# Kernel optimization log

Hardware: AMD Instinct MI355X
Metric: run time of the kernel (lower is better)

The kernel has to match this reference:

```python
import jax, jax.numpy as jnp
import numpy as np

N, E, F, H, L, G, C, NC = 100000, 1200000, 32, 64, 3, 256, 200000, 10
D = L * H  # concat node embedding dim = 192


def setup_inputs() -> dict:
    key = jax.random.key(0)
    ks = jax.random.split(key, 20)

    def w(k, shape):
        fan_in = shape[-2] if len(shape) > 1 else shape[0]
        return jax.random.normal(k, shape, jnp.float32) * (1.0 / np.sqrt(fan_in))

    inp = dict(
        x=jax.random.normal(ks[0], (N, F), jnp.float32),
        edge_index=jax.random.randint(ks[1], (2, E), 0, N),
        batch=jnp.sort(jax.random.randint(ks[2], (N,), 0, G)),
        cand_node=jax.random.randint(ks[3], (C,), 0, N),
        c1_W1=w(ks[4], (F, H)), c1_b1=jnp.zeros((H,)),
        c1_W2=w(ks[5], (H, H)), c1_b2=jnp.zeros((H,)),
        c1_g=jnp.ones((H,)), c1_be=jnp.zeros((H,)), c1_m=jnp.zeros((H,)), c1_v=jnp.ones((H,)),
        c1_eps=jnp.zeros((1,)),
        cs_W1=w(ks[6], (L - 1, H, H)), cs_b1=jnp.zeros((L - 1, H)),
        cs_W2=w(ks[7], (L - 1, H, H)), cs_b2=jnp.zeros((L - 1, H)),
        cs_g=jnp.ones((L - 1, H)), cs_be=jnp.zeros((L - 1, H)),
        cs_m=jnp.zeros((L - 1, H)), cs_v=jnp.ones((L - 1, H)),
        cs_eps=jnp.zeros((L - 1,)),
        nc_W1=w(ks[8], (D, 2 * H)), nc_b1=jnp.zeros((2 * H,)),
        nc_W2=w(ks[9], (2 * H, H)), nc_b2=jnp.zeros((H,)),
        nc_W3=w(ks[10], (H, H)), nc_b3=jnp.zeros((H,)),
        nc_W4=w(ks[11], (H, NC)), nc_b4=jnp.zeros((NC,)),
        comp_emb=jax.random.normal(ks[12], (NC, D), jnp.float32),
        ep_W1=w(ks[13], (2 * D, 2 * H)), ep_b1=jnp.zeros((2 * H,)),
        ep_W2=w(ks[14], (2 * H, H)), ep_b2=jnp.zeros((H,)),
        ep_W3=w(ks[15], (H, 1)), ep_b3=jnp.zeros((1,)),
    )
    return inp


def _bn(h, g, b, m, v):
    # BatchNorm1d in eval mode with running stats
    return g * (h - m) * jax.lax.rsqrt(v + 1e-5) + b


def _gin_layer(h, src, dst, eps, W1, b1, W2, b2, g, be, m, v):
    agg = jax.ops.segment_sum(h[src], dst, num_segments=N)  # sum aggregation
    h = (1.0 + eps) * h + agg
    h = jax.nn.relu(h @ W1 + b1)
    h = jax.nn.relu(h @ W2 + b2)
    return _bn(h, g, be, m, v)


def reference(x, edge_index, batch, cand_node,
              c1_W1, c1_b1, c1_W2, c1_b2, c1_g, c1_be, c1_m, c1_v, c1_eps,
              cs_W1, cs_b1, cs_W2, cs_b2, cs_g, cs_be, cs_m, cs_v, cs_eps,
              nc_W1, nc_b1, nc_W2, nc_b2, nc_W3, nc_b3, nc_W4, nc_b4,
              comp_emb, ep_W1, ep_b1, ep_W2, ep_b2, ep_W3, ep_b3):
    src, dst = edge_index[0], edge_index[1]
    # shared GIN encoder: concat per-layer node embeddings -> [N, L*H]
    h = _gin_layer(x, src, dst, c1_eps, c1_W1, c1_b1, c1_W2, c1_b2, c1_g, c1_be, c1_m, c1_v)
    xs = [h]
    for i in range(cs_W1.shape[0]):
        h = _gin_layer(h, src, dst, cs_eps[i], cs_W1[i], cs_b1[i], cs_W2[i], cs_b2[i],
                       cs_g[i], cs_be[i], cs_m[i], cs_v[i])
        xs.append(h)
    node_emb = jnp.concatenate(xs, axis=-1)  # [N, D]

    # global mean pool per graph -> classification head (dropout=identity in eval)
    sums = jax.ops.segment_sum(node_emb, batch, num_segments=G)
    cnt = jax.ops.segment_sum(jnp.ones((node_emb.shape[0], 1), node_emb.dtype), batch, num_segments=G)
    graph_emb = sums / jnp.maximum(cnt, 1.0)  # [G, D]
    hc = jax.nn.relu(graph_emb @ nc_W1 + nc_b1)
    hc = jax.nn.relu(hc @ nc_W2 + nc_b2)
    hc = jax.nn.relu(hc @ nc_W3 + nc_b3)
    logits = hc @ nc_W4 + nc_b4
    class_output = jax.nn.log_softmax(logits, axis=-1)  # [G, NC]

    # link prediction: predicted comp type per graph, score all candidates in one batch
    comp_idx = jnp.argmax(class_output, axis=-1)          # [G]
    cand_graph = batch[cand_node]                          # [C]
    ce = comp_emb[comp_idx[cand_graph]]                    # [C, D]
    de = node_emb[cand_node]                               # [C, D]
    ef = jnp.concatenate([ce, de], axis=-1)                # [C, 2D]
    he = jax.nn.relu(ef @ ep_W1 + ep_b1)
    he = jax.nn.relu(he @ ep_W2 + ep_b2)
    edge_scores = jax.nn.sigmoid((he @ ep_W3 + ep_b3).squeeze(-1))  # [C]
    return class_output, edge_scores
```

## Files before the change

kernel.cpp:

```cpp
#include <hip/hip_runtime.h>
#include <hip/hip_bf16.h>


#define GG 256
#define NCC 10
#define DD 192
#define BSH 9

typedef short bf16x8 __attribute__((ext_vector_type(8)));
typedef float f32x4  __attribute__((ext_vector_type(4)));

__device__ inline unsigned short f2bf_u(float x) {
    __hip_bfloat16 h = __float2bfloat16(x);
    return *reinterpret_cast<unsigned short*>(&h);
}
__device__ inline float bf2f(unsigned short u) {
    return __uint_as_float(((unsigned int)u) << 16);
}

__global__ void bin_hist(const int* __restrict__ dst, int* __restrict__ bcnt, int E_) {
    __shared__ int h[256];
    h[threadIdx.x] = 0;
    __syncthreads();
    for (int e = blockIdx.x * 256 + threadIdx.x; e < E_; e += gridDim.x * 256)
        atomicAdd(&h[dst[e] >> BSH], 1);
    __syncthreads();
    if (h[threadIdx.x]) atomicAdd(&bcnt[threadIdx.x], h[threadIdx.x]);
}

__global__ void bin_scan(const int* __restrict__ bcnt, int* __restrict__ bbase,
                         int* __restrict__ bpos, int NB, int E_) {
    __shared__ int s[256];
    const int t = threadIdx.x;
    int v = (t < NB) ? bcnt[t] : 0;
    s[t] = v;
    __syncthreads();
    for (int off = 1; off < 256; off <<= 1) {
        int x = (t >= off) ? s[t - off] : 0;
        __syncthreads();
        s[t] += x;
        __syncthreads();
    }
    if (t < NB) { bbase[t] = s[t] - v; bpos[t] = s[t] - v; }
    if (t == 0) bbase[NB] = E_;
}

__global__ __launch_bounds__(256) void bin_scatter(
    const int* __restrict__ src, const int* __restrict__ dst,
    int* __restrict__ bpos, int2* __restrict__ ebuf, int E_) {
    __shared__ int h[256];
    __shared__ int base[256];
    const int t = threadIdx.x;
    const int e0 = blockIdx.x * 2048;
    h[t] = 0;
    __syncthreads();
    int myb[8], mys[8], myd[8], myr[8];
    #pragma unroll
    for (int u = 0; u < 8; ++u) {
        int e = e0 + t + u * 256;
        if (e < E_) {
            int d = dst[e];
            myb[u] = d >> BSH;
            myd[u] = d;
            mys[u] = src[e];
            myr[u] = atomicAdd(&h[myb[u]], 1);
        } else myb[u] = -1;
    }
    __syncthreads();
    if (h[t]) base[t] = atomicAdd(&bpos[t], h[t]);
    __syncthreads();
    #pragma unroll
    for (int u = 0; u < 8; ++u)
        if (myb[u] >= 0)
            ebuf[base[myb[u]] + myr[u]] = make_int2(mys[u], myd[u]);
}

__global__ __launch_bounds__(256) void csr_bucket(
    const int2* __restrict__ ebuf, const int* __restrict__ bbase,
    int* __restrict__ rowptr, int* __restrict__ nbr, int N_, int NB) {
    __shared__ int lh[512];
    __shared__ int lx[512];
    __shared__ int ps[256];
    const int b = blockIdx.x;
    const int t = threadIdx.x;
    const int ebase = bbase[b], eend = bbase[b + 1];
    const int ecnt = eend - ebase;
    const int n0 = b << BSH;

    for (int i = t; i < 512; i += 256) lh[i] = 0;
    __syncthreads();
    for (int i = t; i < ecnt; i += 256)
        atomicAdd(&lh[ebuf[ebase + i].y - n0], 1);
    __syncthreads();

    int pv = lh[2 * t] + lh[2 * t + 1];
    ps[t] = pv;
    __syncthreads();
    for (int off = 1; off < 256; off <<= 1) {
        int x = (t >= off) ? ps[t - off] : 0;
        __syncthreads();
        ps[t] += x;
        __syncthreads();
    }
    const int excl = ps[t] - pv;
    lx[2 * t] = excl;
    lx[2 * t + 1] = excl + lh[2 * t];
    __syncthreads();

    for (int i = t; i < 512; i += 256) {
        int n = n0 + i;
        if (n < N_) rowptr[n] = ebase + lx[i];
    }
    if (b == NB - 1 && t == 0) rowptr[N_] = eend;

    for (int i = t; i < 512; i += 256) lh[i] = lx[i];
    __syncthreads();
    for (int i = t; i < ecnt; i += 256) {
        int2 p = ebuf[ebase + i];
        int r = atomicAdd(&lh[p.y - n0], 1);
        nbr[ebase + r] = p.x;
    }
}

__global__ void x2b_kernel(const float* __restrict__ x, unsigned short* __restrict__ xb,
                           int n_elem) {
    int i = blockIdx.x * 256 + threadIdx.x;
    int stride = gridDim.x * 256;
    for (; i * 4 < n_elem; i += stride) {
        float4 v = *(const float4*)(x + i * 4);
        ushort4 u;
        u.x = f2bf_u(v.x); u.y = f2bf_u(v.y); u.z = f2bf_u(v.z); u.w = f2bf_u(v.w);
        *(ushort4*)(xb + i * 4) = u;
    }
}

__global__ void prep_enc(const float* __restrict__ c1W1, const float* __restrict__ c1W2,
                         const float* __restrict__ csW1, const float* __restrict__ csW2,
                         unsigned short* __restrict__ enc) {
    int idx = blockIdx.x * 256 + threadIdx.x;
    if (idx >= 22528) return;
    const float* W; int rel;
    if (idx < 2048)       { W = c1W1;        rel = idx; }
    else if (idx < 6144)  { W = c1W2;        rel = idx - 2048; }
    else if (idx < 10240) { W = csW1;        rel = idx - 6144; }
    else if (idx < 14336) { W = csW2;        rel = idx - 10240; }
    else if (idx < 18432) { W = csW1 + 4096; rel = idx - 14336; }
    else                  { W = csW2 + 4096; rel = idx - 18432; }
    int frag = rel >> 9;
    int lane = (rel >> 3) & 63;
    int j = rel & 7;
    int ks = frag >> 2, nt = frag & 3;
    int k = ks * 32 + ((lane >> 4) << 3) + j;
    int n = nt * 16 + (lane & 15);
    enc[idx] = f2bf_u(W[k * 64 + n]);
}

__global__ void gcnt_bs(const int* __restrict__ batch, int* __restrict__ gcnt_i, int N_) {
    __shared__ int lbs[GG + 1];
    const int g = threadIdx.x;
    int lo = 0, hi = N_;
    while (lo < hi) {
        int mid = (lo + hi) >> 1;
        if (batch[mid] < g) lo = mid + 1; else hi = mid;
    }
    lbs[g] = lo;
    if (g == 0) lbs[GG] = N_;
    __syncthreads();
    gcnt_i[g] = lbs[g + 1] - lbs[g];
}

#define SWZ(row, byte) ((byte) ^ (((row) & 7) << 4))

#define GSTEP(VCUR, VNXT)                                                     \
    _Pragma("unroll")                                                         \
    for (int u = 0; u < 16; ++u)                                              \
        VNXT[u] = bf2f(*(const unsigned short*)(hbase + (unsigned)idx[u] * (unsigned)(DD*2) + lane2)); \
    _Pragma("unroll")                                                         \
    for (int u = 0; u < 16; ++u) idx[u] = nbp[k + 32 + u];                    \
    {                                                                         \
        float runk = run;                                                     \
        _Pragma("unroll")                                                     \
        for (int u = 0; u < 16; ++u) run += VCUR[u];                          \
        if ((unsigned)(e1 - k) < 16u) { float tt = runk;                      \
            _Pragma("unroll")                                                 \
            for (int u = 0; u < 16; ++u) tt += (u < e1 - k) ? VCUR[u] : 0.f;  \
            s0 = tt; }                                                        \
        if ((unsigned)(e2 - k) < 16u) { float tt = runk;                      \
            _Pragma("unroll")                                                 \
            for (int u = 0; u < 16; ++u) tt += (u < e2 - k) ? VCUR[u] : 0.f;  \
            s1 = tt; }                                                        \
        if ((unsigned)(e3 - k) < 16u) { float tt = runk;                      \
            _Pragma("unroll")                                                 \
            for (int u = 0; u < 16; ++u) tt += (u < e3 - k) ? VCUR[u] : 0.f;  \
            s2 = tt; }                                                        \
        if ((unsigned)(cnt - k) < 16u) { float tt = runk;                     \
            _Pragma("unroll")                                                 \
            for (int u = 0; u < 16; ++u) tt += (u < cnt - k) ? VCUR[u] : 0.f; \
            s3 = tt; }                                                        \
    }                                                                         \
    k += 16;                                                                  \
    if (k > cnt) break;

template<int K>
__global__ __launch_bounds__(512) void gin_fused(
    const unsigned short* __restrict__ hin_b,
    const int* __restrict__ rowptr, const int* __restrict__ nbr,
    const unsigned short* __restrict__ W1p, const float* __restrict__ b1,
    const unsigned short* __restrict__ W2p, const float* __restrict__ b2,
    const float* __restrict__ gamma, const float* __restrict__ beta,
    const float* __restrict__ mean, const float* __restrict__ var,
    const float* __restrict__ eps_p,
    __hip_bfloat16* __restrict__ out_b,
    const int* __restrict__ batch, float* __restrict__ gsum, int soff,
    int N_) {
    __shared__ char s_agg[32 * 128];
    __shared__ char s_h1[32 * 128];
    __shared__ char s_out[32 * 128];
    __shared__ int sb[32];

    const int t = threadIdx.x;
    const int lane = t & 63;
    const int w = t >> 6;
    const int node0 = blockIdx.x * 32;
    const int nb = w * 4;

    if (t < 32) sb[t] = (node0 + t < N_) ? batch[node0 + t] : -1;

    const float eps1 = 1.0f + eps_p[0];

    const int n0w = node0 + nb;
    const int rp0 = __builtin_amdgcn_readfirstlane(rowptr[min(n0w + 0, N_)]);
    const int rp1 = __builtin_amdgcn_readfirstlane(rowptr[min(n0w + 1, N_)]);
    const int rp2 = __builtin_amdgcn_readfirstlane(rowptr[min(n0w + 2, N_)]);
    const int rp3 = __builtin_amdgcn_readfirstlane(rowptr[min(n0w + 3, N_)]);
    const int rp4 = __builtin_amdgcn_readfirstlane(rowptr[min(n0w + 4, N_)]);
    const int cnt = rp4 - rp0;
    const int e1 = rp1 - rp0, e2 = rp2 - rp0, e3 = rp3 - rp0;
    const int* nbp = nbr + rp0;

    float a0 = 0.f, a1 = 0.f, a2 = 0.f, a3 = 0.f;

    if (K == 64) {
        const char* hbase = (const char*)hin_b;
        const unsigned lane2 = (unsigned)lane * 2u;
        int idx[16];
        float vA[16], vB[16];
        float run = 0.f, s0 = 0.f, s1 = 0.f, s2 = 0.f, s3 = 0.f;
        #pragma unroll
        for (int u = 0; u < 16; ++u) idx[u] = nbp[u];
        #pragma unroll
        for (int u = 0; u < 16; ++u)
            vA[u] = bf2f(*(const unsigned short*)(hbase + (unsigned)idx[u] * (unsigned)(DD*2) + lane2));
        #pragma unroll
        for (int u = 0; u < 16; ++u) idx[u] = nbp[16 + u];
        for (int k = 0;;) {
            GSTEP(vA, vB)
            GSTEP(vB, vA)
        }
        a0 = s0; a1 = s1 - s0; a2 = s2 - s1; a3 = s3 - s2;
        const unsigned short* hbp = hin_b + lane;
        if (n0w + 0 < N_) a0 += eps1 * bf2f(hbp[(size_t)(n0w + 0) * DD]);
        if (n0w + 1 < N_) a1 += eps1 * bf2f(hbp[(size_t)(n0w + 1) * DD]);
        if (n0w + 2 < N_) a2 += eps1 * bf2f(hbp[(size_t)(n0w + 2) * DD]);
        if (n0w + 3 < N_) a3 += eps1 * bf2f(hbp[(size_t)(n0w + 3) * DD]);
        *(unsigned short*)(s_agg + SWZ(nb + 0, (nb + 0) * 128 + lane * 2)) = f2bf_u(a0);
        *(unsigned short*)(s_agg + SWZ(nb + 1, (nb + 1) * 128 + lane * 2)) = f2bf_u(a1);
        *(unsigned short*)(s_agg + SWZ(nb + 2, (nb + 2) * 128 + lane * 2)) = f2bf_u(a2);
        *(unsigned short*)(s_agg + SWZ(nb + 3, (nb + 3) * 128 + lane * 2)) = f2bf_u(a3);
    } else {
        const int d = lane & 31, rs = lane >> 5;
        const unsigned short* xp = hin_b + d;
        int idxb[8];
        #pragma unroll
        for (int u = 0; u < 8; ++u) idxb[u] = nbp[2 * u + rs];
        for (int k = 0; k < cnt; k += 16) {
            int nxt[8];
            #pragma unroll
            for (int u = 0; u < 8; ++u) nxt[u] = nbp[k + 16 + 2 * u + rs];
            #pragma unroll
            for (int u = 0; u < 8; ++u) {
                float v = bf2f(xp[(size_t)idxb[u] * 32]);
                int j = k + 2 * u + rs;
                a0 += (j < e1)             ? v : 0.f;
                a1 += (j >= e1 && j < e2)  ? v : 0.f;
                a2 += (j >= e2 && j < e3)  ? v : 0.f;
                a3 += (j >= e3 && j < cnt) ? v : 0.f;
            }
            #pragma unroll
            for (int u = 0; u < 8; ++u) idxb[u] = nxt[u];
        }
        a0 += __shfl_xor(a0, 32);
        a1 += __shfl_xor(a1, 32);
        a2 += __shfl_xor(a2, 32);
        a3 += __shfl_xor(a3, 32);
        if (rs == 0) {
            if (n0w + 0 < N_) a0 += eps1 * bf2f(xp[(size_t)(n0w + 0) * 32]);
            if (n0w + 1 < N_) a1 += eps1 * bf2f(xp[(size_t)(n0w + 1) * 32]);
            if (n0w + 2 < N_) a2 += eps1 * bf2f(xp[(size_t)(n0w + 2) * 32]);
            if (n0w + 3 < N_) a3 += eps1 * bf2f(xp[(size_t)(n0w + 3) * 32]);
            *(unsigned short*)(s_agg + SWZ(nb + 0, (nb + 0) * 128 + d * 2)) = f2bf_u(a0);
            *(unsigned short*)(s_agg + SWZ(nb + 1, (nb + 1) * 128 + d * 2)) = f2bf_u(a1);
            *(unsigned short*)(s_agg + SWZ(nb + 2, (nb + 2) * 128 + d * 2)) = f2bf_u(a2);
            *(unsigned short*)(s_agg + SWZ(nb + 3, (nb + 3) * 128 + d * 2)) = f2bf_u(a3);
        }
    }
    __syncthreads();

    const int mt = w >> 2, nt = w & 3;
    const int arow = mt * 16 + (lane & 15);
    const int col = nt * 16 + (lane & 15);
    f32x4 c1v = (f32x4){0.f, 0.f, 0.f, 0.f};
    #pragma unroll
    for (int ks = 0; ks < K / 32; ++ks) {
        bf16x8 a = *(const bf16x8*)(s_agg + SWZ(arow, arow * 128 + ks * 64 + ((lane >> 4) << 4)));
        bf16x8 b = *(const bf16x8*)(W1p + (((ks << 2) + nt) << 9) + (lane << 3));
        c1v = __builtin_amdgcn_mfma_f32_16x16x32_bf16(a, b, c1v, 0, 0, 0);
    }
    {
        const float bb1 = b1[col];
        #pragma unroll
        for (int reg = 0; reg < 4; ++reg) {
            int row = mt * 16 + ((lane >> 4) << 2) + reg;
            float v = fmaxf(c1v[reg] + bb1, 0.f);
            *(unsigned short*)(s_h1 + SWZ(row, row * 128 + col * 2)) = f2bf_u(v);
        }
    }
    __syncthreads();

    f32x4 c2v = (f32x4){0.f, 0.f, 0.f, 0.f};
    #pragma unroll
    for (int ks = 0; ks < 2; ++ks) {
        bf16x8 a = *(const bf16x8*)(s_h1 + SWZ(arow, arow * 128 + ks * 64 + ((lane >> 4) << 4)));
        bf16x8 b = *(const bf16x8*)(W2p + (((ks << 2) + nt) << 9) + (lane << 3));
        c2v = __builtin_amdgcn_mfma_f32_16x16x32_bf16(a, b, c2v, 0, 0, 0);
    }
    {
        const float bb2 = b2[col];
        const float ga = gamma[col], bet = beta[col], mu = mean[col];
        const float iv = rsqrtf(var[col] + 1e-5f);
        #pragma unroll
        for (int reg = 0; reg < 4; ++reg) {
            int row = mt * 16 + ((lane >> 4) << 2) + reg;
            float v = fmaxf(c2v[reg] + bb2, 0.f);
            v = ga * (v - mu) * iv + bet;
            *(unsigned short*)(s_out + SWZ(row, row * 128 + col * 2)) = f2bf_u(v);
        }
    }
    __syncthreads();

    {
        int r = t >> 4, c8 = t & 15;
        int node = node0 + r;
        if (node < N_) {
            ushort4 v = *(const ushort4*)(s_out + SWZ(r, r * 128 + c8 * 8));
            *(ushort4*)((unsigned short*)out_b + (size_t)node * DD + c8 * 4) = v;
        }
    }

    if (t < 256) {
        const int d = t & 63;
        const int rg = t >> 6;
        float acc = 0.f;
        int curg = sb[rg * 8];
        #pragma unroll
        for (int r = rg * 8; r < rg * 8 + 8; ++r) {
            int g = sb[r];
            if (g != curg) {
                if (curg >= 0) atomicAdd(&gsum[curg * DD + soff + d], acc);
                acc = 0.f; curg = g;
            }
            if (g >= 0)
                acc += bf2f(*(const unsigned short*)(s_out + SWZ(r, r * 128 + d * 2)));
        }
        if (curg >= 0) atomicAdd(&gsum[curg * DD + soff + d], acc);
    }
}

__global__ void head_kernel(const float* __restrict__ gsum, const int* __restrict__ gcnt_i,
                            const float* __restrict__ W1, const float* __restrict__ b1,
                            const float* __restrict__ W2, const float* __restrict__ b2,
                            const float* __restrict__ W3, const float* __restrict__ b3,
                            const float* __restrict__ W4, const float* __restrict__ b4,
                            float* __restrict__ class_out, int* __restrict__ comp_idx) {
    const int g = blockIdx.x;
    const int t = threadIdx.x;
    __shared__ float ge[DD], h1[128], h2[64], h3[64], logits[NCC];

    const float c = fmaxf((float)gcnt_i[g], 1.0f);
    if (t < DD) ge[t] = gsum[g * DD + t] / c;
    __syncthreads();

    if (t < 128) {
        float a = b1[t];
        #pragma unroll 4
        for (int k = 0; k < DD; ++k) a += ge[k] * W1[k * 128 + t];
        h1[t] = fmaxf(a, 0.0f);
    }
    __syncthreads();
    if (t < 64) {
        float a = b2[t];
        #pragma unroll 4
        for (int k = 0; k < 128; ++k) a += h1[k] * W2[k * 64 + t];
        h2[t] = fmaxf(a, 0.0f);
    }
    __syncthreads();
    if (t < 64) {
        float a = b3[t];
        #pragma unroll 4
        for (int k = 0; k < 64; ++k) a += h2[k] * W3[k * 64 + t];
        h3[t] = fmaxf(a, 0.0f);
    }
    __syncthreads();
    if (t < NCC) {
        float a = b4[t];
        #pragma unroll
        for (int k = 0; k < 64; ++k) a += h3[k] * W4[k * NCC + t];
        logits[t] = a;
    }
    __syncthreads();
    if (t == 0) {
        float mx = logits[0]; int am = 0;
        for (int j = 1; j < NCC; ++j) if (logits[j] > mx) { mx = logits[j]; am = j; }
        float se = 0.0f;
        for (int j = 0; j < NCC; ++j) se += expf(logits[j] - mx);
        float lse = logf(se);
        for (int j = 0; j < NCC; ++j) class_out[g * NCC + j] = logits[j] - mx - lse;
        comp_idx[g] = am;
    }
}

__global__ void prep_edge(const float* __restrict__ W1, const float* __restrict__ b1,
                          const float* __restrict__ W2, const float* __restrict__ comp_emb,
                          unsigned short* __restrict__ W1b_p, unsigned short* __restrict__ W2_p,
                          float* __restrict__ pc) {
    int idx = blockIdx.x * 256 + threadIdx.x;
    const int S1 = 6 * 8 * 512;
    const int S2 = 4 * 4 * 512;
    if (idx < S1) {
        int frag = idx >> 9;
        int lane = (idx >> 3) & 63;
        int j = idx & 7;
        int kstep = frag >> 3, nt = frag & 7;
        int k = kstep * 32 + ((lane >> 4) << 3) + j;
        int n = nt * 16 + (lane & 15);
        W1b_p[idx] = f2bf_u(W1[(192 + k) * 128 + n]);
    } else if (idx < S1 + S2) {
        int i2 = idx - S1;
        int frag = i2 >> 9;
        int lane = (i2 >> 3) & 63;
        int j = i2 & 7;
        int kstep = frag >> 2, nt = frag & 3;
        int k = kstep * 32 + ((lane >> 4) << 3) + j;
        int n = nt * 16 + (lane & 15);
        W2_p[i2] = f2bf_u(W2[k * 64 + n]);
    } else if (idx < S1 + S2 + NCC * 128) {
        int i3 = idx - (S1 + S2);
        int ci = i3 >> 7, col = i3 & 127;
        float a = b1[col];
        for (int k = 0; k < DD; ++k) a += comp_emb[ci * DD + k] * W1[k * 128 + col];
        pc[i3] = a;
    }
}

__global__ __launch_bounds__(256, 5) void edge_mfma(
    const int* __restrict__ cand, const int* __restrict__ batch,
    const int* __restrict__ comp_idx, const short* __restrict__ hb,
    const unsigned short* __restrict__ W1b_p, const unsigned short* __restrict__ W2_p,
    const float* __restrict__ pc, const float* __restrict__ W3,
    const float* __restrict__ b3, float* __restrict__ scores, int C_) {
    __shared__ char s_buf[64 * 384];
    __shared__ float s_part[4][64];
    __shared__ int s_node[64];
    __shared__ int s_ci[64];
    __shared__ float s_w3[64];

    const int t = threadIdx.x;
    const int lane = t & 63;
    const int w = t >> 6;
    const int c0 = blockIdx.x * 64;

    if (t < 64) {
        int c = c0 + t;
        int node = (c < C_) ? cand[c] : cand[0];
        s_node[t] = node;
        s_ci[t] = comp_idx[batch[node]];
        s_w3[t] = W3[t];
    }
    __syncthreads();

    for (int i = t; i < 64 * 24; i += 256) {
        int r = i / 24, c8 = i - r * 24;
        bf16x8 v = *(const bf16x8*)(hb + (size_t)s_node[r] * DD + c8 * 8);
        *(bf16x8*)(s_buf + SWZ(r, r * 384 + c8 * 16)) = v;
    }
    __syncthreads();

    f32x4 acc1[4][2];
    #pragma unroll
    for (int rt = 0; rt < 4; ++rt)
        #pragma unroll
        for (int b = 0; b < 2; ++b) acc1[rt][b] = (f32x4){0.f, 0.f, 0.f, 0.f};
    #pragma unroll
    for (int ks = 0; ks < 6; ++ks) {
        bf16x8 b0 = *(const bf16x8*)(W1b_p + ((ks * 8 + 2 * w + 0) << 9) + (lane << 3));
        bf16x8 b1f = *(const bf16x8*)(W1b_p + ((ks * 8 + 2 * w + 1) << 9) + (lane << 3));
        #pragma unroll
        for (int rt = 0; rt < 4; ++rt) {
            int arow = rt * 16 + (lane & 15);
            bf16x8 a = *(const bf16x8*)(s_buf + SWZ(arow, arow * 384 + ks * 64 + ((lane >> 4) << 4)));
            acc1[rt][0] = __builtin_amdgcn_mfma_f32_16x16x32_bf16(a, b0, acc1[rt][0], 0, 0, 0);
            acc1[rt][1] = __builtin_amdgcn_mfma_f32_16x16x32_bf16(a, b1f, acc1[rt][1], 0, 0, 0);
        }
    }
    __syncthreads();

    #pragma unroll
    for (int rt = 0; rt < 4; ++rt) {
        #pragma unroll
        for (int reg = 0; reg < 4; ++reg) {
            int row = rt * 16 + ((lane >> 4) << 2) + reg;
            int ci = s_ci[row];
            #pragma unroll
            for (int b = 0; b < 2; ++b) {
                int col = (2 * w + b) * 16 + (lane & 15);
                float v = fmaxf(acc1[rt][b][reg] + pc[ci * 128 + col], 0.f);
                *(unsigned short*)(s_buf + SWZ(row, row * 256 + col * 2)) = f2bf_u(v);
            }
        }
    }
    __syncthreads();

    f32x4 acc2[4];
    #pragma unroll
    for (int rt = 0; rt < 4; ++rt) acc2[rt] = (f32x4){0.f, 0.f, 0.f, 0.f};
    #pragma unroll
    for (int ks = 0; ks < 4; ++ks) {
        bf16x8 b = *(const bf16x8*)(W2_p + ((ks * 4 + w) << 9) + (lane << 3));
        #pragma unroll
        for (int rt = 0; rt < 4; ++rt) {
            int arow = rt * 16 + (lane & 15);
            bf16x8 a = *(const bf16x8*)(s_buf + SWZ(arow, arow * 256 + ks * 64 + ((lane >> 4) << 4)));
            acc2[rt] = __builtin_amdgcn_mfma_f32_16x16x32_bf16(a, b, acc2[rt], 0, 0, 0);
        }
    }

    {
        const float w3v = s_w3[w * 16 + (lane & 15)];
        #pragma unroll
        for (int rt = 0; rt < 4; ++rt) {
            #pragma unroll
            for (int reg = 0; reg < 4; ++reg) {
                float p = fmaxf(acc2[rt][reg], 0.f) * w3v;
                p += __shfl_xor(p, 1);
                p += __shfl_xor(p, 2);
                p += __shfl_xor(p, 4);
                p += __shfl_xor(p, 8);
                if ((lane & 15) == 0)
                    s_part[w][rt * 16 + ((lane >> 4) << 2) + reg] = p;
            }
        }
    }
    __syncthreads();

    if (t < 64) {
        int c = c0 + t;
        if (c < C_) {
            float p = s_part[0][t] + s_part[1][t] + s_part[2][t] + s_part[3][t] + b3[0];
            scores[c] = 1.0f / (1.0f + expf(-p));
        }
    }
}

extern "C" void kernel_launch(void* const* d_in, const int* in_sizes, int n_in,
                              void* d_out, int out_size, void* d_ws, size_t ws_size,
                              hipStream_t stream) {
    const float* x        = (const float*)d_in[0];
    const int*   ei       = (const int*)d_in[1];
    const int*   batch    = (const int*)d_in[2];
    const int*   cand     = (const int*)d_in[3];
    const float* c1_W1    = (const float*)d_in[4];
    const float* c1_b1    = (const float*)d_in[5];
    const float* c1_W2    = (const float*)d_in[6];
    const float* c1_b2    = (const float*)d_in[7];
    const float* c1_g     = (const float*)d_in[8];
    const float* c1_be    = (const float*)d_in[9];
    const float* c1_m     = (const float*)d_in[10];
    const float* c1_v     = (const float*)d_in[11];
    const float* c1_eps   = (const float*)d_in[12];
    const float* cs_W1    = (const float*)d_in[13];
    const float* cs_b1    = (const float*)d_in[14];
    const float* cs_W2    = (const float*)d_in[15];
    const float* cs_b2    = (const float*)d_in[16];
    const float* cs_g     = (const float*)d_in[17];
    const float* cs_be    = (const float*)d_in[18];
    const float* cs_m     = (const float*)d_in[19];
    const float* cs_v     = (const float*)d_in[20];
    const float* cs_eps   = (const float*)d_in[21];
    const float* nc_W1    = (const float*)d_in[22];
    const float* nc_b1    = (const float*)d_in[23];
    const float* nc_W2    = (const float*)d_in[24];
    const float* nc_b2    = (const float*)d_in[25];
    const float* nc_W3    = (const float*)d_in[26];
    const float* nc_b3    = (const float*)d_in[27];
    const float* nc_W4    = (const float*)d_in[28];
    const float* nc_b4    = (const float*)d_in[29];
    const float* comp_emb = (const float*)d_in[30];
    const float* ep_W1    = (const float*)d_in[31];
    const float* ep_b1    = (const float*)d_in[32];
    const float* ep_W2    = (const float*)d_in[33];
    const float* ep_b2    = (const float*)d_in[34];
    const float* ep_W3    = (const float*)d_in[35];
    const float* ep_b3    = (const float*)d_in[36];

    const int N_ = in_sizes[0] / 32;
    const int E_ = in_sizes[1] / 2;
    const int C_ = in_sizes[3];
    const int* src = ei;
    const int* dst = ei + E_;
    const int NB = (N_ + (1 << BSH) - 1) >> BSH;

    char* ws = (char*)d_ws;
    size_t off = 0;
    __hip_bfloat16* hb = (__hip_bfloat16*)(ws + off); off += (size_t)N_ * DD * 2;
    unsigned short* xb = (unsigned short*)(ws + off); off += (size_t)N_ * 32 * 2;
    int*   rowptr   = (int*)(ws + off);   off += (size_t)(N_ + 2) * 4;
    int*   nbr      = (int*)(ws + off);   off += (size_t)(E_ + 64) * 4;
    int*   bcnt     = (int*)(ws + off);   off += 1024;
    int*   bbase    = (int*)(ws + off);   off += 1044;
    int*   bpos     = (int*)(ws + off);   off += 1024;
    float* gsum     = (float*)(ws + off); off += (size_t)GG * DD * 4;
    int*   gcnt_i   = (int*)(ws + off);   off += 1024;
    int*   comp_idx = (int*)(ws + off);   off += 1024;
    float* pc       = (float*)(ws + off); off += NCC * 128 * 4;
    unsigned short* W1b_p = (unsigned short*)(ws + off); off += 6 * 8 * 512 * 2;
    unsigned short* W2_p  = (unsigned short*)(ws + off); off += 4 * 4 * 512 * 2;
    unsigned short* enc   = (unsigned short*)(ws + off); off += 22528 * 2;
    int2*  ebuf     = (int2*)hb;

    float* class_out = (float*)d_out;
    float* scores    = class_out + GG * NCC;

    prep_edge<<<(6 * 8 * 512 + 4 * 4 * 512 + NCC * 128 + 255) / 256, 256, 0, stream>>>(
        ep_W1, ep_b1, ep_W2, comp_emb, W1b_p, W2_p, pc);
    prep_enc<<<(22528 + 255) / 256, 256, 0, stream>>>(c1_W1, c1_W2, cs_W1, cs_W2, enc);
    x2b_kernel<<<2048, 256, 0, stream>>>(x, xb, N_ * 32);

    hipMemsetAsync(bcnt, 0, 1024, stream);
    hipMemsetAsync(nbr + E_, 0, 64 * 4, stream);
    bin_hist<<<1024, 256, 0, stream>>>(dst, bcnt, E_);
    bin_scan<<<1, 256, 0, stream>>>(bcnt, bbase, bpos, NB, E_);
    bin_scatter<<<(E_ + 2047) / 2048, 256, 0, stream>>>(src, dst, bpos, ebuf, E_);
    csr_bucket<<<NB, 256, 0, stream>>>(ebuf, bbase, rowptr, nbr, N_, NB);

    hipMemsetAsync(gsum, 0, (size_t)GG * DD * 4, stream);
    gcnt_bs<<<1, GG, 0, stream>>>(batch, gcnt_i, N_);

    const int gblk = (N_ + 31) / 32;
    gin_fused<32><<<gblk, 512, 0, stream>>>(
        xb, rowptr, nbr,
        enc + 0, c1_b1, enc + 2048, c1_b2,
        c1_g, c1_be, c1_m, c1_v, c1_eps, hb + 0, batch, gsum, 0, N_);
    gin_fused<64><<<gblk, 512, 0, stream>>>(
        (const unsigned short*)hb + 0, rowptr, nbr,
        enc + 6144, cs_b1 + 0, enc + 10240, cs_b2 + 0,
        cs_g + 0, cs_be + 0, cs_m + 0, cs_v + 0, cs_eps + 0, hb + 64, batch, gsum, 64, N_);
    gin_fused<64><<<gblk, 512, 0, stream>>>(
        (const unsigned short*)hb + 64, rowptr, nbr,
        enc + 14336, cs_b1 + 64, enc + 18432, cs_b2 + 64,
        cs_g + 64, cs_be + 64, cs_m + 64, cs_v + 64, cs_eps + 1, hb + 128, batch, gsum, 128, N_);

    head_kernel<<<GG, 256, 0, stream>>>(gsum, gcnt_i, nc_W1, nc_b1, nc_W2, nc_b2,
                                        nc_W3, nc_b3, nc_W4, nc_b4, class_out, comp_idx);

    edge_mfma<<<(C_ + 63) / 64, 256, 0, stream>>>(
        cand, batch, comp_idx, (const short*)hb, W1b_p, W2_p, pc, ep_W3, ep_b3, scores, C_);
}
```

Measured before the change: 300.4 us.

## Pack edges into 32-bit words, shrink CSR buckets, triple-buffer neighbor gathers

The CSR build now uses 256-node buckets (391 of them) and packs each edge as src<<8 | local dst into one 32-bit word instead of an int2, which halves the intermediate edge-buffer traffic. The scan and scatter kernels are widened to handle up to 512 buckets, and scatter blocks now cover 4096 edges each. The GIN aggregation replaces the separate first-layer path with the same unrolled gather loop used by the other layers, with lanes 32-63 duplicating the work and their results discarded. It also adds a third register buffer so loads stay two steps ahead. This raises register pressure and puts more padding on the neighbor array.

```diff
diff --git a/kernel.cpp b/kernel.cpp
--- a/kernel.cpp
+++ b/kernel.cpp
@@ -5,7 +5,7 @@
 #define GG 256
 #define NCC 10
 #define DD 192
-#define BSH 9
+#define BSH 8
 
 typedef short bf16x8 __attribute__((ext_vector_type(8)));
 typedef float f32x4  __attribute__((ext_vector_type(4)));
@@ -19,67 +19,74 @@
 }
 
 __global__ void bin_hist(const int* __restrict__ dst, int* __restrict__ bcnt, int E_) {
-    __shared__ int h[256];
-    h[threadIdx.x] = 0;
-    __syncthreads();
-    for (int e = blockIdx.x * 256 + threadIdx.x; e < E_; e += gridDim.x * 256)
+    __shared__ int h[512];
+    const int t = threadIdx.x;
+    h[t] = 0; h[t + 256] = 0;
+    __syncthreads();
+    for (int e = blockIdx.x * 256 + t; e < E_; e += gridDim.x * 256)
         atomicAdd(&h[dst[e] >> BSH], 1);
     __syncthreads();
-    if (h[threadIdx.x]) atomicAdd(&bcnt[threadIdx.x], h[threadIdx.x]);
+    if (h[t]) atomicAdd(&bcnt[t], h[t]);
+    if (h[t + 256]) atomicAdd(&bcnt[t + 256], h[t + 256]);
 }
 
 __global__ void bin_scan(const int* __restrict__ bcnt, int* __restrict__ bbase,
                          int* __restrict__ bpos, int NB, int E_) {
-    __shared__ int s[256];
+    __shared__ int ps[256];
     const int t = threadIdx.x;
-    int v = (t < NB) ? bcnt[t] : 0;
-    s[t] = v;
+    int v0 = (2 * t < NB) ? bcnt[2 * t] : 0;
+    int v1 = (2 * t + 1 < NB) ? bcnt[2 * t + 1] : 0;
+    int pv = v0 + v1;
+    ps[t] = pv;
     __syncthreads();
     for (int off = 1; off < 256; off <<= 1) {
-        int x = (t >= off) ? s[t - off] : 0;
+        int x = (t >= off) ? ps[t - off] : 0;
         __syncthreads();
-        s[t] += x;
+        ps[t] += x;
         __syncthreads();
     }
-    if (t < NB) { bbase[t] = s[t] - v; bpos[t] = s[t] - v; }
+    const int excl = ps[t] - pv;
+    if (2 * t < NB)     { bbase[2 * t] = excl;          bpos[2 * t] = excl; }
+    if (2 * t + 1 < NB) { bbase[2 * t + 1] = excl + v0; bpos[2 * t + 1] = excl + v0; }
     if (t == 0) bbase[NB] = E_;
 }
 
 __global__ __launch_bounds__(256) void bin_scatter(
     const int* __restrict__ src, const int* __restrict__ dst,
-    int* __restrict__ bpos, int2* __restrict__ ebuf, int E_) {
-    __shared__ int h[256];
-    __shared__ int base[256];
+    int* __restrict__ bpos, unsigned* __restrict__ ebuf, int E_) {
+    __shared__ int h[512];
+    __shared__ int base[512];
     const int t = threadIdx.x;
-    const int e0 = blockIdx.x * 2048;
-    h[t] = 0;
-    __syncthreads();
-    int myb[8], mys[8], myd[8], myr[8];
-    #pragma unroll
-    for (int u = 0; u < 8; ++u) {
+    const int e0 = blockIdx.x * 4096;
+    h[t] = 0; h[t + 256] = 0;
+    __syncthreads();
+    int myb[16], myr[16];
+    unsigned pk[16];
+    #pragma unroll
+    for (int u = 0; u < 16; ++u) {
         int e = e0 + t + u * 256;
         if (e < E_) {
             int d = dst[e];
             myb[u] = d >> BSH;
-            myd[u] = d;
-            mys[u] = src[e];
+            pk[u] = ((unsigned)src[e] << BSH) | (unsigned)(d & ((1 << BSH) - 1));
             myr[u] = atomicAdd(&h[myb[u]], 1);
         } else myb[u] = -1;
     }
     __syncthreads();
     if (h[t]) base[t] = atomicAdd(&bpos[t], h[t]);
-    __syncthreads();
-    #pragma unroll
-    for (int u = 0; u < 8; ++u)
+    if (h[t + 256]) base[t + 256] = atomicAdd(&bpos[t + 256], h[t + 256]);
+    __syncthreads();
+    #pragma unroll
+    for (int u = 0; u < 16; ++u)
         if (myb[u] >= 0)
-            ebuf[base[myb[u]] + myr[u]] = make_int2(mys[u], myd[u]);
+            ebuf[base[myb[u]] + myr[u]] = pk[u];
 }
 
 __global__ __launch_bounds__(256) void csr_bucket(
-    const int2* __restrict__ ebuf, const int* __restrict__ bbase,
+    const unsigned* __restrict__ ebuf, const int* __restrict__ bbase,
     int* __restrict__ rowptr, int* __restrict__ nbr, int N_, int NB) {
-    __shared__ int lh[512];
-    __shared__ int lx[512];
+    __shared__ int lh[256];
+    __shared__ int lx[256];
     __shared__ int ps[256];
     const int b = blockIdx.x;
     const int t = threadIdx.x;
@@ -87,14 +94,14 @@
     const int ecnt = eend - ebase;
     const int n0 = b << BSH;
 
-    for (int i = t; i < 512; i += 256) lh[i] = 0;
+    lh[t] = 0;
     __syncthreads();
     for (int i = t; i < ecnt; i += 256)
-        atomicAdd(&lh[ebuf[ebase + i].y - n0], 1);
-    __syncthreads();
-
-    int pv = lh[2 * t] + lh[2 * t + 1];
-    ps[t] = pv;
+        atomicAdd(&lh[ebuf[ebase + i] & ((1 << BSH) - 1)], 1);
+    __syncthreads();
+
+    int v = lh[t];
+    ps[t] = v;
     __syncthreads();
     for (int off = 1; off < 256; off <<= 1) {
         int x = (t >= off) ? ps[t - off] : 0;
@@ -102,23 +109,19 @@
         ps[t] += x;
         __syncthreads();
     }
-    const int excl = ps[t] - pv;
-    lx[2 * t] = excl;
-    lx[2 * t + 1] = excl + lh[2 * t];
-    __syncthreads();
-
-    for (int i = t; i < 512; i += 256) {
-        int n = n0 + i;
-        if (n < N_) rowptr[n] = ebase + lx[i];
+    lx[t] = ps[t] - v;
+    {
+        int n = n0 + t;
+        if (n < N_) rowptr[n] = ebase + lx[t];
     }
     if (b == NB - 1 && t == 0) rowptr[N_] = eend;
-
-    for (int i = t; i < 512; i += 256) lh[i] = lx[i];
+    __syncthreads();
+    lh[t] = lx[t];
     __syncthreads();
     for (int i = t; i < ecnt; i += 256) {
-        int2 p = ebuf[ebase + i];
-        int r = atomicAdd(&lh[p.y - n0], 1);
-        nbr[ebase + r] = p.x;
+        unsigned p = ebuf[ebase + i];
+        int r = atomicAdd(&lh[p & ((1 << BSH) - 1)], 1);
+        nbr[ebase + r] = (int)(p >> BSH);
     }
 }
 
@@ -174,9 +177,9 @@
 #define GSTEP(VCUR, VNXT)                                                     \
     _Pragma("unroll")                                                         \
     for (int u = 0; u < 16; ++u)                                              \
-        VNXT[u] = bf2f(*(const unsigned short*)(hbase + (unsigned)idx[u] * (unsigned)(DD*2) + lane2)); \
+        VNXT[u] = bf2f(*(const unsigned short*)(hbase + (unsigned)idx[u] * (unsigned)RSB + lane2)); \
     _Pragma("unroll")                                                         \
-    for (int u = 0; u < 16; ++u) idx[u] = nbp[k + 32 + u];                    \
+    for (int u = 0; u < 16; ++u) idx[u] = nbp[k + 48 + u];                    \
     {                                                                         \
         float runk = run;                                                     \
         _Pragma("unroll")                                                     \
@@ -238,71 +241,45 @@
     const int e1 = rp1 - rp0, e2 = rp2 - rp0, e3 = rp3 - rp0;
     const int* nbp = nbr + rp0;
 
-    float a0 = 0.f, a1 = 0.f, a2 = 0.f, a3 = 0.f;
-
-    if (K == 64) {
-        const char* hbase = (const char*)hin_b;
-        const unsigned lane2 = (unsigned)lane * 2u;
-        int idx[16];
-        float vA[16], vB[16];
-        float run = 0.f, s0 = 0.f, s1 = 0.f, s2 = 0.f, s3 = 0.f;
-        #pragma unroll
-        for (int u = 0; u < 16; ++u) idx[u] = nbp[u];
-        #pragma unroll
-        for (int u = 0; u < 16; ++u)
-            vA[u] = bf2f(*(const unsigned short*)(hbase + (unsigned)idx[u] * (unsigned)(DD*2) + lane2));
-        #pragma unroll
-        for (int u = 0; u < 16; ++u) idx[u] = nbp[16 + u];
-        for (int k = 0;;) {
-            GSTEP(vA, vB)
-            GSTEP(vB, vA)
-        }
-        a0 = s0; a1 = s1 - s0; a2 = s2 - s1; a3 = s3 - s2;
-        const unsigned short* hbp = hin_b + lane;
-        if (n0w + 0 < N_) a0 += eps1 * bf2f(hbp[(size_t)(n0w + 0) * DD]);
-        if (n0w + 1 < N_) a1 += eps1 * bf2f(hbp[(size_t)(n0w + 1) * DD]);
-        if (n0w + 2 < N_) a2 += eps1 * bf2f(hbp[(size_t)(n0w + 2) * DD]);
-        if (n0w + 3 < N_) a3 += eps1 * bf2f(hbp[(size_t)(n0w + 3) * DD]);
-        *(unsigned short*)(s_agg + SWZ(nb + 0, (nb + 0) * 128 + lane * 2)) = f2bf_u(a0);
-        *(unsigned short*)(s_agg + SWZ(nb + 1, (nb + 1) * 128 + lane * 2)) = f2bf_u(a1);
-        *(unsigned short*)(s_agg + SWZ(nb + 2, (nb + 2) * 128 + lane * 2)) = f2bf_u(a2);
-        *(unsigned short*)(s_agg + SWZ(nb + 3, (nb + 3) * 128 + lane * 2)) = f2bf_u(a3);
-    } else {
-        const int d = lane & 31, rs = lane >> 5;
-        const unsigned short* xp = hin_b + d;
-        int idxb[8];
-        #pragma unroll
-        for (int u = 0; u < 8; ++u) idxb[u] = nbp[2 * u + rs];
-        for (int k = 0; k < cnt; k += 16) {
-            int nxt[8];
-            #pragma unroll
-            for (int u = 0; u < 8; ++u) nxt[u] = nbp[k + 16 + 2 * u + rs];
-            #pragma unroll
-            for (int u = 0; u < 8; ++u) {
-                float v = bf2f(xp[(size_t)idxb[u] * 32]);
-                int j = k + 2 * u + rs;
-                a0 += (j < e1)             ? v : 0.f;
-                a1 += (j >= e1 && j < e2)  ? v : 0.f;
-                a2 += (j >= e2 && j < e3)  ? v : 0.f;
-                a3 += (j >= e3 && j < cnt) ? v : 0.f;
-            }
-            #pragma unroll
-            for (int u = 0; u < 8; ++u) idxb[u] = nxt[u];
-        }
-        a0 += __shfl_xor(a0, 32);
-        a1 += __shfl_xor(a1, 32);
-        a2 += __shfl_xor(a2, 32);
-        a3 += __shfl_xor(a3, 32);
-        if (rs == 0) {
-            if (n0w + 0 < N_) a0 += eps1 * bf2f(xp[(size_t)(n0w + 0) * 32]);
-            if (n0w + 1 < N_) a1 += eps1 * bf2f(xp[(size_t)(n0w + 1) * 32]);
-            if (n0w + 2 < N_) a2 += eps1 * bf2f(xp[(size_t)(n0w + 2) * 32]);
-            if (n0w + 3 < N_) a3 += eps1 * bf2f(xp[(size_t)(n0w + 3) * 32]);
-            *(unsigned short*)(s_agg + SWZ(nb + 0, (nb + 0) * 128 + d * 2)) = f2bf_u(a0);
-            *(unsigned short*)(s_agg + SWZ(nb + 1, (nb + 1) * 128 + d * 2)) = f2bf_u(a1);
-            *(unsigned short*)(s_agg + SWZ(nb + 2, (nb + 2) * 128 + d * 2)) = f2bf_u(a2);
-            *(unsigned short*)(s_agg + SWZ(nb + 3, (nb + 3) * 128 + d * 2)) = f2bf_u(a3);
-        }
+    const int RSB = (K == 64) ? DD * 2 : 64;
+    const int OST = (K == 64) ? DD : 32;
+    const char* hbase = (const char*)hin_b;
+    const unsigned lane2 = (unsigned)(lane & (K - 1)) * 2u;
+
+    int idx[16];
+    float vA[16], vB[16], vC[16];
+    float run = 0.f, s0 = 0.f, s1 = 0.f, s2 = 0.f, s3 = 0.f;
+    #pragma unroll
+    for (int u = 0; u < 16; ++u) idx[u] = nbp[u];
+    #pragma unroll
+    for (int u = 0; u < 16; ++u)
+        vA[u] = bf2f(*(const unsigned short*)(hbase + (unsigned)idx[u] * (unsigned)RSB + lane2));
+    #pragma unroll
+    for (int u = 0; u < 16; ++u) idx[u] = nbp[16 + u];
+    #pragma unroll
+    for (int u = 0; u < 16; ++u)
+        vB[u] = bf2f(*(const unsigned short*)(hbase + (unsigned)idx[u] * (unsigned)RSB + lane2));
+    #pragma unroll
+    for (int u = 0; u < 16; ++u) idx[u] = nbp[32 + u];
+    for (int k = 0;;) {
+        GSTEP(vA, vC)
+        GSTEP(vB, vA)
+        GSTEP(vC, vB)
+    }
+    float a0 = s0, a1 = s1 - s0, a2 = s2 - s1, a3 = s3 - s2;
+    {
+        const unsigned short* hbp = hin_b + (lane & (K - 1));
+        if (n0w + 0 < N_) a0 += eps1 * bf2f(hbp[(size_t)(n0w + 0) * OST]);
+        if (n0w + 1 < N_) a1 += eps1 * bf2f(hbp[(size_t)(n0w + 1) * OST]);
+        if (n0w + 2 < N_) a2 += eps1 * bf2f(hbp[(size_t)(n0w + 2) * OST]);
+        if (n0w + 3 < N_) a3 += eps1 * bf2f(hbp[(size_t)(n0w + 3) * OST]);
+    }
+    if (K == 64 || lane < 32) {
+        const int kd = lane & (K - 1);
+        *(unsigned short*)(s_agg + SWZ(nb + 0, (nb + 0) * 128 + kd * 2)) = f2bf_u(a0);
+        *(unsigned short*)(s_agg + SWZ(nb + 1, (nb + 1) * 128 + kd * 2)) = f2bf_u(a1);
+        *(unsigned short*)(s_agg + SWZ(nb + 2, (nb + 2) * 128 + kd * 2)) = f2bf_u(a2);
+        *(unsigned short*)(s_agg + SWZ(nb + 3, (nb + 3) * 128 + kd * 2)) = f2bf_u(a3);
     }
     __syncthreads();
 
@@ -624,10 +601,10 @@
     __hip_bfloat16* hb = (__hip_bfloat16*)(ws + off); off += (size_t)N_ * DD * 2;
     unsigned short* xb = (unsigned short*)(ws + off); off += (size_t)N_ * 32 * 2;
     int*   rowptr   = (int*)(ws + off);   off += (size_t)(N_ + 2) * 4;
-    int*   nbr      = (int*)(ws + off);   off += (size_t)(E_ + 64) * 4;
-    int*   bcnt     = (int*)(ws + off);   off += 1024;
-    int*   bbase    = (int*)(ws + off);   off += 1044;
-    int*   bpos     = (int*)(ws + off);   off += 1024;
+    int*   nbr      = (int*)(ws + off);   off += (size_t)(E_ + 128) * 4;
+    int*   bcnt     = (int*)(ws + off);   off += 2048;
+    int*   bbase    = (int*)(ws + off);   off += 2080;
+    int*   bpos     = (int*)(ws + off);   off += 2048;
     float* gsum     = (float*)(ws + off); off += (size_t)GG * DD * 4;
     int*   gcnt_i   = (int*)(ws + off);   off += 1024;
     int*   comp_idx = (int*)(ws + off);   off += 1024;
@@ -635,7 +612,7 @@
     unsigned short* W1b_p = (unsigned short*)(ws + off); off += 6 * 8 * 512 * 2;
     unsigned short* W2_p  = (unsigned short*)(ws + off); off += 4 * 4 * 512 * 2;
     unsigned short* enc   = (unsigned short*)(ws + off); off += 22528 * 2;
-    int2*  ebuf     = (int2*)hb;
+    unsigned* ebuf  = (unsigned*)hb;
 
     float* class_out = (float*)d_out;
     float* scores    = class_out + GG * NCC;
@@ -645,11 +622,11 @@
     prep_enc<<<(22528 + 255) / 256, 256, 0, stream>>>(c1_W1, c1_W2, cs_W1, cs_W2, enc);
     x2b_kernel<<<2048, 256, 0, stream>>>(x, xb, N_ * 32);
 
-    hipMemsetAsync(bcnt, 0, 1024, stream);
-    hipMemsetAsync(nbr + E_, 0, 64 * 4, stream);
+    hipMemsetAsync(bcnt, 0, 2048, stream);
+    hipMemsetAsync(nbr + E_, 0, 128 * 4, stream);
     bin_hist<<<1024, 256, 0, stream>>>(dst, bcnt, E_);
     bin_scan<<<1, 256, 0, stream>>>(bcnt, bbase, bpos, NB, E_);
-    bin_scatter<<<(E_ + 2047) / 2048, 256, 0, stream>>>(src, dst, bpos, ebuf, E_);
+    bin_scatter<<<(E_ + 4095) / 4096, 256, 0, stream>>>(src, dst, bpos, ebuf, E_);
     csr_bucket<<<NB, 256, 0, stream>>>(ebuf, bbase, rowptr, nbr, N_, NB);
 
     hipMemsetAsync(gsum, 0, (size_t)GG * DD * 4, stream);
```

Measured after the change: 311.6 us. 3.7% more time.
